# Kernel tuning notes

Measured on AMD Instinct MI355X. Metric: run time of the kernel, lower is better.

Reference implementation:

```python
import jax, jax.numpy as jnp
import numpy as np

N = {'QENT': 20000, 'CENT': 50000, 'SPAN': 40000, 'SENT': 40000}
E = 250000
IN_DIM, HID = 256, 128
NEG_SLOPE = 0.2  # GATConv default negative_slope
RELS = [('QENT', 'SPAN'), ('QENT', 'SENT'), ('CENT', 'SENT'), ('SPAN', 'CENT'), ('CENT', 'CENT')]
ENAMES = ['e_qent_span', 'e_qent_sent', 'e_cent_sent', 'e_span_cent', 'e_cent_cooccur']


def setup_inputs() -> dict:
    key = jax.random.key(0)
    ks = jax.random.split(key, 20)
    inp = {}
    for i, t in enumerate(['QENT', 'CENT', 'SPAN', 'SENT']):
        inp['x_' + t] = jax.random.normal(ks[i], (N[t], IN_DIM), jnp.float32)
    for i, (nm, (s, d)) in enumerate(zip(ENAMES, RELS)):
        k1, k2 = jax.random.split(ks[4 + i])
        src = jax.random.randint(k1, (E,), 0, N[s])
        dst = jax.random.randint(k2, (E,), 0, N[d])
        inp[nm] = jnp.stack([src, dst]).astype(jnp.int32)
    inp['lin_W'] = jax.random.normal(ks[10], (4, IN_DIM, HID), jnp.float32) / np.sqrt(IN_DIM).astype(np.float32)
    inp['lin_b'] = jnp.zeros((4, HID), jnp.float32)
    inp['conv_Ws'] = jax.random.normal(ks[11], (2, 5, HID, HID), jnp.float32) / np.sqrt(HID).astype(np.float32)
    inp['conv_Wd'] = jax.random.normal(ks[12], (2, 5, HID, HID), jnp.float32) / np.sqrt(HID).astype(np.float32)
    inp['conv_as'] = jax.random.normal(ks[13], (2, 5, HID), jnp.float32) / np.sqrt(HID).astype(np.float32)
    inp['conv_ad'] = jax.random.normal(ks[14], (2, 5, HID), jnp.float32) / np.sqrt(HID).astype(np.float32)
    inp['conv_b'] = jnp.zeros((2, 5, HID), jnp.float32)
    inp['out_W'] = jax.random.normal(ks[15], (HID, 1), jnp.float32) / np.sqrt(HID).astype(np.float32)
    inp['out_b'] = jnp.zeros((1,), jnp.float32)
    return inp


def _gat(x_src, x_dst, edge, Ws, Wd, a_s, a_d, b, n_dst):
    """PyG GATConv, heads=1, concat=True, add_self_loops=False, bipartite lin_src/lin_dst."""
    hs = x_src @ Ws                       # [Ns, H]
    hd = x_dst @ Wd                       # [Nd, H]
    src, dst = edge[0], edge[1]
    e = jax.nn.leaky_relu((hs @ a_s)[src] + (hd @ a_d)[dst], NEG_SLOPE)  # [E]
    m = jax.ops.segment_max(e, dst, num_segments=n_dst)
    m = jnp.where(jnp.isfinite(m), m, 0.0)
    ex = jnp.exp(e - m[dst])
    denom = jax.ops.segment_sum(ex, dst, num_segments=n_dst)
    alpha = ex / (denom[dst] + 1e-16)     # segment softmax (PyG adds 1e-16)
    out = jax.ops.segment_sum(alpha[:, None] * hs[src], dst, num_segments=n_dst)
    return out + b


def _forward(x_QENT, x_CENT, x_SPAN, x_SENT,
             e_qent_span, e_qent_sent, e_cent_sent, e_span_cent, e_cent_cooccur,
             lin_W, lin_b, conv_Ws, conv_Wd, conv_as, conv_ad, conv_b, out_W, out_b):
    # per-type input projection (pyg Linear has bias)
    x = {'QENT': x_QENT @ lin_W[0] + lin_b[0],
         'CENT': x_CENT @ lin_W[1] + lin_b[1],
         'SPAN': x_SPAN @ lin_W[2] + lin_b[2],
         'SENT': x_SENT @ lin_W[3] + lin_b[3]}
    for l in range(2):
        p = lambda r: (conv_Ws[l, r], conv_Wd[l, r], conv_as[l, r], conv_ad[l, r], conv_b[l, r])
        span = _gat(x['QENT'], x['SPAN'], e_qent_span, *p(0), N['SPAN'])
        sent = (_gat(x['QENT'], x['SENT'], e_qent_sent, *p(1), N['SENT'])
                + _gat(x['CENT'], x['SENT'], e_cent_sent, *p(2), N['SENT']))  # HeteroConv aggr='sum'
        cent = (_gat(x['SPAN'], x['CENT'], e_span_cent, *p(3), N['CENT'])
                + _gat(x['CENT'], x['CENT'], e_cent_cooccur, *p(4), N['CENT']))
        x = {'QENT': x['QENT'],  # QENT has no incoming edges; carried through so layer 2 can use it as source
             'SPAN': jax.nn.relu(span),
             'SENT': jax.nn.relu(sent),
             'CENT': jax.nn.relu(cent)}
    return (x['SPAN'] @ out_W + out_b)[:, 0]  # squeeze(-1) -> [N_SPAN]


def reference(x_QENT, x_CENT, x_SPAN, x_SENT,
              e_qent_span, e_qent_sent, e_cent_sent, e_span_cent, e_cent_cooccur,
              lin_W, lin_b, conv_Ws, conv_Wd, conv_as, conv_ad, conv_b, out_W, out_b):
    return _forward(x_QENT, x_CENT, x_SPAN, x_SENT,
                    e_qent_span, e_qent_sent, e_cent_sent, e_span_cent, e_cent_cooccur,
                    lin_W, lin_b, conv_Ws, conv_Wd, conv_as, conv_ad, conv_b, out_W, out_b)
```

## Files before the change

### kernel.cpp

```cpp
#include <hip/hip_runtime.h>
#include <hip/hip_fp16.h>

#define IN_DIM 256
#define HID 128
#define ELLW 16
#define OVF_CAP 32768

using bf16x8 = __attribute__((ext_vector_type(8))) short;
using f32x4 = __attribute__((ext_vector_type(4))) float;

struct h8 { __half2 a, b, c, d; };

__device__ __forceinline__ unsigned short f2bf(float f) {
    unsigned u = __float_as_uint(f);
    u += 0x7fffu + ((u >> 16) & 1u);
    return (unsigned short)(u >> 16);
}

template <int CTRL>
__device__ __forceinline__ float dpp_rot(float x) {
    return __int_as_float(
        __builtin_amdgcn_update_dpp(0, __float_as_int(x), CTRL, 0xf, 0xf, false));
}
__device__ __forceinline__ float rsum16(float x) {
    x += dpp_rot<0x121>(x);
    x += dpp_rot<0x122>(x);
    x += dpp_rot<0x124>(x);
    x += dpp_rot<0x128>(x);
    return x;
}
__device__ __forceinline__ float rmax16(float x) {
    x = fmaxf(x, dpp_rot<0x121>(x));
    x = fmaxf(x, dpp_rot<0x122>(x));
    x = fmaxf(x, dpp_rot<0x124>(x));
    x = fmaxf(x, dpp_rot<0x128>(x));
    return x;
}

__device__ __forceinline__ float lrelu(float t) { return t > 0.f ? t : 0.2f * t; }

__device__ __forceinline__ void accum8(f32x4& a0, f32x4& a1, float a, const h8& hv) {
    const float2 f0 = __half22float2(hv.a);
    const float2 f1 = __half22float2(hv.b);
    const float2 f2 = __half22float2(hv.c);
    const float2 f3 = __half22float2(hv.d);
    a0[0] += a * f0.x; a0[1] += a * f0.y;
    a0[2] += a * f1.x; a0[3] += a * f1.y;
    a1[0] += a * f2.x; a1[1] += a * f2.y;
    a1[2] += a * f3.x; a1[3] += a * f3.y;
}

__device__ __forceinline__ float epilogue16(const f32x4& a0, const f32x4& a1,
                                            const float* __restrict__ bias,
                                            const float* __restrict__ dvec, int sl) {
    const f32x4 bb0 = *reinterpret_cast<const f32x4*>(bias + sl * 8);
    const f32x4 bb1 = *reinterpret_cast<const f32x4*>(bias + sl * 8 + 4);
    const f32x4 d0 = *reinterpret_cast<const f32x4*>(dvec + sl * 8);
    const f32x4 d1 = *reinterpret_cast<const f32x4*>(dvec + sl * 8 + 4);
    float q = 0.f;
#pragma unroll
    for (int i = 0; i < 4; ++i) {
        q += fmaxf(a0[i] + bb0[i], 0.f) * d0[i];
        q += fmaxf(a1[i] + bb1[i], 0.f) * d1[i];
    }
    return rsum16(q);
}

__global__ __launch_bounds__(256) void setup_k(const float* __restrict__ lin_W,
                                               const float* __restrict__ lin_b,
                                               const float* __restrict__ conv_Ws,
                                               const float* __restrict__ Wd,
                                               const float* __restrict__ adv,
                                               short* __restrict__ wt0,
                                               short* __restrict__ wt1,
                                               float* __restrict__ bc,
                                               float* __restrict__ wd_out,
                                               float* __restrict__ v2,
                                               float* __restrict__ c2,
                                               int* __restrict__ deg,
                                               int* __restrict__ ell,
                                               int* __restrict__ ovf_cnt, int NS, int zd) {
    const int b = blockIdx.x;
    if (b < 256) {
        const int idx = b * 256 + threadIdx.x;
        const int l = idx >> 15;
        const int rem = idx & 32767;
        const int k = rem >> 7;
        const int n = rem & 127;
        const float* lw = lin_W + (size_t)k * HID;
        const float* cw = conv_Ws + (size_t)(l * 5) * HID * HID + n;
        float s = 0.f;
#pragma unroll 4
        for (int m = 0; m < HID; ++m) s += lw[m] * cw[(size_t)m * HID];
        short* wt = l ? wt1 : wt0;
        wt[((k >> 3) << 10) + (n << 3) + (k & 7)] = (short)f2bf(s);
    } else if (b == 256) {
        const int t = threadIdx.x;
        const int l = t >> 7;
        const int n = t & 127;
        const float* cw = conv_Ws + (size_t)(l * 5) * HID * HID + n;
        float s = 0.f;
#pragma unroll 4
        for (int m = 0; m < HID; ++m) s += lin_b[m] * cw[(size_t)m * HID];
        bc[t] = s;
        if (t == 0) ovf_cnt[0] = 0;
    } else if (b == 257) {
        __shared__ float wd1s[HID];
        const int t = threadIdx.x;
        const int l = t >> 7, j = t & 127;
        const float* w = Wd + ((size_t)(l * 5) * HID + j) * HID;
        const float* a = adv + (size_t)(l * 5) * HID;
        float s = 0.f;
        for (int k = 0; k < HID; k += 4) {
            const float4 wv = *reinterpret_cast<const float4*>(w + k);
            const float4 av = *reinterpret_cast<const float4*>(a + k);
            s += wv.x * av.x + wv.y * av.y + wv.z * av.z + wv.w * av.w;
        }
        wd_out[t] = s;
        if (l == 0) wd1s[j] = s;
        __syncthreads();
        const float* wr = lin_W + 2 * (size_t)IN_DIM * HID + (size_t)t * HID;
        float p = 0.f;
        for (int k = 0; k < HID; k += 4) {
            const float4 wv = *reinterpret_cast<const float4*>(wr + k);
            p += wv.x * wd1s[k] + wv.y * wd1s[k + 1] + wv.z * wd1s[k + 2] +
                 wv.w * wd1s[k + 3];
        }
        v2[t] = p;
        if (t == 0) {
            const float* br = lin_b + 2 * HID;
            float q = 0.f;
            for (int k = 0; k < HID; ++k) q += br[k] * wd1s[k];
            c2[0] = q;
        }
    } else if (b < 258 + zd) {
        const int i4 = ((b - 258) * 256 + threadIdx.x) * 4;
        if (i4 + 4 <= NS) {
            *reinterpret_cast<int4*>(deg + i4) = make_int4(0, 0, 0, 0);
        } else {
            for (int i = i4; i < NS; ++i) deg[i] = 0;
        }
    } else {
        const int total = NS * ELLW;
        const int i4 = ((b - 258 - zd) * 256 + threadIdx.x) * 4;
        if (i4 + 4 <= total) *reinterpret_cast<int4*>(ell + i4) = make_int4(0, 0, 0, 0);
    }
}

__global__ __launch_bounds__(256) void build_gemm_k(
    const int* __restrict__ src, const int* __restrict__ dst, int E,
    int* __restrict__ deg, int* __restrict__ ell, int2* __restrict__ ovf,
    int* __restrict__ ovf_cnt, const float* __restrict__ A,
    const short* __restrict__ Wt0, const short* __restrict__ Wt1,
    const float* __restrict__ bc, __half* __restrict__ hs,
    float2* __restrict__ as12, const float* __restrict__ a1v,
    const float* __restrict__ a2v, int N, int eb) {
    if ((int)blockIdx.x < eb) {
        const int e = blockIdx.x * 256 + threadIdx.x;
        if (e < E) {
            const int d = dst[e], s = src[e];
            const int pos = atomicAdd(deg + d, 1);
            if (pos < ELLW) {
                ell[(size_t)d * ELLW + pos] = s;
            } else {
                const int oi = atomicAdd(ovf_cnt, 1);
                if (oi < OVF_CAP) ovf[oi] = make_int2(d, s);
            }
        }
        return;
    }
    const int bid = (int)blockIdx.x - eb;
    const int tid = threadIdx.x;
    const int w = tid >> 6;
    const int lane = tid & 63;
    const int m16 = lane & 15;
    const int kg = lane >> 4;

    const int arow = bid * 64 + w * 16 + m16;
    const bool ok = arow < N;

    f32x4 acc[16];
#pragma unroll
    for (int j = 0; j < 16; ++j) acc[j] = (f32x4){0.f, 0.f, 0.f, 0.f};

    for (int k0 = 0; k0 < IN_DIM; k0 += 32) {
        bf16x8 af = {0, 0, 0, 0, 0, 0, 0, 0};
        if (ok) {
            const float* ap = A + (size_t)arow * IN_DIM + k0 + kg * 8;
            const float4 f0 = *reinterpret_cast<const float4*>(ap);
            const float4 f1 = *reinterpret_cast<const float4*>(ap + 4);
            af[0] = (short)f2bf(f0.x); af[1] = (short)f2bf(f0.y);
            af[2] = (short)f2bf(f0.z); af[3] = (short)f2bf(f0.w);
            af[4] = (short)f2bf(f1.x); af[5] = (short)f2bf(f1.y);
            af[6] = (short)f2bf(f1.z); af[7] = (short)f2bf(f1.w);
        }
        const int boff = ((k0 >> 3) + kg) << 10;
        const short* b0 = Wt0 + boff;
        const short* b1 = Wt1 + boff;
#pragma unroll
        for (int j = 0; j < 8; ++j) {
            const bf16x8 bf0 = *reinterpret_cast<const bf16x8*>(b0 + ((j * 16 + m16) << 3));
            acc[j] = __builtin_amdgcn_mfma_f32_16x16x32_bf16(af, bf0, acc[j], 0, 0, 0);
            const bf16x8 bf1 = *reinterpret_cast<const bf16x8*>(b1 + ((j * 16 + m16) << 3));
            acc[j + 8] = __builtin_amdgcn_mfma_f32_16x16x32_bf16(af, bf1, acc[j + 8], 0, 0, 0);
        }
    }

    const int rbase = bid * 64 + w * 16 + kg * 4;
    float p1[4] = {0.f, 0.f, 0.f, 0.f};
    float p2[4] = {0.f, 0.f, 0.f, 0.f};
#pragma unroll
    for (int j = 0; j < 8; ++j) {
        const int col = j * 16 + m16;
        const float b0v = bc[col];
        const float b1v = bc[128 + col];
        const float a1 = a1v[col];
        const float a2 = a2v[col];
        const int so = j * 32 + ((m16 >> 3) << 4) + (m16 & 7);
#pragma unroll
        for (int r = 0; r < 4; ++r) {
            const int row = rbase + r;
            const float v1 = acc[j][r] + b0v;
            const float v2v = acc[j + 8][r] + b1v;
            if (row < N) {
                hs[(size_t)row * 256 + so] = __float2half(v1);
                hs[(size_t)row * 256 + so + 8] = __float2half(v2v);
            }
            p1[r] += v1 * a1;
            p2[r] += v2v * a2;
        }
    }
#pragma unroll
    for (int r = 0; r < 4; ++r) {
        p1[r] = rsum16(p1[r]);
        p2[r] = rsum16(p2[r]);
    }
    if (m16 == 0)
#pragma unroll
        for (int r = 0; r < 4; ++r) {
            const int row = rbase + r;
            if (row < N) as12[row] = make_float2(p1[r], p2[r]);
        }
}

__global__ __launch_bounds__(256, 4) void gat_fused_k(
    const int* __restrict__ deg_arr, const int* __restrict__ ell,
    const int2* __restrict__ ovf, const int* __restrict__ ovf_cnt_p,
    const float* __restrict__ x_span, const float* __restrict__ v2,
    const float* __restrict__ c2, const float2* __restrict__ as12,
    const __half* __restrict__ hs, const float* __restrict__ b1,
    const float* __restrict__ wd2v, const float* __restrict__ b2,
    const float* __restrict__ outW, const float* __restrict__ outb,
    float* __restrict__ out, int Ndst) {
    const int gidx = blockIdx.x * blockDim.x + threadIdx.x;
    const int row = gidx >> 4;
    const int sl = threadIdx.x & 15;
    const int grp = threadIdx.x & 48;
    if (row >= Ndst) return;

    const int deg = deg_arr[row];
    const int ce = ell[(size_t)row * ELLW + sl];

    float p = 0.f;
    const float* xr = x_span + (size_t)row * IN_DIM + sl * 16;
    const float* vr = v2 + sl * 16;
#pragma unroll
    for (int i = 0; i < 4; ++i) {
        const float4 xv = *reinterpret_cast<const float4*>(xr + i * 4);
        const float4 vv = *reinterpret_cast<const float4*>(vr + i * 4);
        p += xv.x * vv.x + xv.y * vv.y + xv.z * vv.z + xv.w * vv.w;
    }
    const float ad1 = rsum16(p) + c2[0];

    const float2 asv = as12[ce];
    const float a1c = asv.x;
    const float a2c = asv.y;

    h8 h1[8], h2[8];
#pragma unroll
    for (int i = 0; i < 8; ++i) {
        const int s = __shfl(ce, grp | i, 64);
        const __half* hb = hs + (size_t)s * 256 + sl * 16;
        h1[i] = *reinterpret_cast<const h8*>(hb);
        h2[i] = *reinterpret_cast<const h8*>(hb + 8);
    }

    if (deg <= ELLW) {
        const float ex1 = (sl < deg) ? __expf(lrelu(a1c + ad1)) : 0.f;
        const float al1 = ex1 / (rsum16(ex1) + 1e-16f);

        f32x4 acc0 = {0.f, 0.f, 0.f, 0.f}, acc1 = {0.f, 0.f, 0.f, 0.f};
#pragma unroll
        for (int i = 0; i < 8; ++i) {
            const float a = __shfl(al1, grp | i, 64);
            accum8(acc0, acc1, a, h1[i]);
        }
        for (int i = 8; i < deg; ++i) {
            const int s = __shfl(ce, grp | i, 64);
            const float a = __shfl(al1, grp | i, 64);
            const h8 hv = *reinterpret_cast<const h8*>(hs + (size_t)s * 256 + sl * 16);
            accum8(acc0, acc1, a, hv);
        }
        const float ad2 = epilogue16(acc0, acc1, b1, wd2v, sl);

        const float ex2 = (sl < deg) ? __expf(lrelu(a2c + ad2)) : 0.f;
        const float al2 = ex2 / (rsum16(ex2) + 1e-16f);

        f32x4 bcc0 = {0.f, 0.f, 0.f, 0.f}, bcc1 = {0.f, 0.f, 0.f, 0.f};
#pragma unroll
        for (int i = 0; i < 8; ++i) {
            const float a = __shfl(al2, grp | i, 64);
            accum8(bcc0, bcc1, a, h2[i]);
        }
        for (int i = 8; i < deg; ++i) {
            const int s = __shfl(ce, grp | i, 64);
            const float a = __shfl(al2, grp | i, 64);
            const h8 hv = *reinterpret_cast<const h8*>(hs + (size_t)s * 256 + sl * 16 + 8);
            accum8(bcc0, bcc1, a, hv);
        }
        const float q = epilogue16(bcc0, bcc1, b2, outW, sl);
        if (sl == 0) out[row] = q + outb[0];
    } else {
        int oc = *ovf_cnt_p;
        if (oc > OVF_CAP) oc = OVF_CAP;
        float ad = ad1;
#pragma unroll
        for (int layer = 0; layer < 2; ++layer) {
            const float ac = layer ? a2c : a1c;
            const int ho = layer ? 8 : 0;
            const float* bias = layer ? b2 : b1;
            const float* dvec = layer ? outW : wd2v;

            float te = lrelu(ac + ad);
            float m = rmax16(te);
            for (int i = 0; i < oc; ++i) {
                const int2 o = ovf[i];
                if (o.x == row) {
                    const float2 oas = as12[o.y];
                    m = fmaxf(m, lrelu((layer ? oas.y : oas.x) + ad));
                }
            }
            const float ex = __expf(te - m);
            float dsum = rsum16(ex);
            for (int i = 0; i < oc; ++i) {
                const int2 o = ovf[i];
                if (o.x == row) {
                    const float2 oas = as12[o.y];
                    dsum += __expf(lrelu((layer ? oas.y : oas.x) + ad) - m);
                }
            }
            const float inv = 1.f / (dsum + 1e-16f);
            const float al = ex * inv;

            f32x4 acc0 = {0.f, 0.f, 0.f, 0.f}, acc1 = {0.f, 0.f, 0.f, 0.f};
#pragma unroll
            for (int i = 0; i < 16; ++i) {
                const int s = __shfl(ce, grp | i, 64);
                const float a = __shfl(al, grp | i, 64);
                const h8 hv =
                    *reinterpret_cast<const h8*>(hs + (size_t)s * 256 + sl * 16 + ho);
                accum8(acc0, acc1, a, hv);
            }
            for (int i = 0; i < oc; ++i) {
                const int2 o = ovf[i];
                if (o.x == row) {
                    const float2 oas = as12[o.y];
                    const float a = __expf(lrelu((layer ? oas.y : oas.x) + ad) - m) * inv;
                    const h8 hv =
                        *reinterpret_cast<const h8*>(hs + (size_t)o.y * 256 + sl * 16 + ho);
                    accum8(acc0, acc1, a, hv);
                }
            }
            const float q = epilogue16(acc0, acc1, bias, dvec, sl);
            if (layer == 0) {
                ad = q;
            } else if (sl == 0) {
                out[row] = q + outb[0];
            }
        }
    }
}

extern "C" void kernel_launch(void* const* d_in, const int* in_sizes, int n_in,
                              void* d_out, int out_size, void* d_ws, size_t ws_size,
                              hipStream_t stream) {
    const float* x_qent = (const float*)d_in[0];
    const float* x_span = (const float*)d_in[2];
    const int* e_qs = (const int*)d_in[4];
    const float* lin_W = (const float*)d_in[9];
    const float* lin_b = (const float*)d_in[10];
    const float* conv_Ws = (const float*)d_in[11];
    const float* conv_Wd = (const float*)d_in[12];
    const float* conv_as = (const float*)d_in[13];
    const float* conv_ad = (const float*)d_in[14];
    const float* conv_b = (const float*)d_in[15];
    const float* out_W = (const float*)d_in[16];
    const float* out_b = (const float*)d_in[17];

    const int NQ = in_sizes[0] / IN_DIM;
    const int NS = in_sizes[2] / IN_DIM;
    const int E = in_sizes[4] / 2;
    const int* srcp = e_qs;
    const int* dstp = e_qs + E;
    (void)n_in; (void)out_size;

    float* ws = (float*)d_ws;
    size_t off = 0;
    auto alloc = [&](size_t n) {
        n = (n + 3) & ~(size_t)3;
        float* p = ws + off;
        off += n;
        return p;
    };
    __half* hs = (__half*)alloc((size_t)NQ * 128);
    float2* as12 = (float2*)alloc(2 * (size_t)NQ);
    float* wd2 = alloc(2 * HID);
    float* v2 = alloc(IN_DIM);
    float* c2 = alloc(1);
    float* bc = alloc(2 * HID);
    int* deg = (int*)alloc(NS);
    int* ell = (int*)alloc((size_t)NS * ELLW);
    int2* ovf = (int2*)alloc(2 * OVF_CAP);
    int* ovf_cnt = (int*)alloc(1);
    short* wt0 = (short*)alloc(IN_DIM * HID / 2);
    short* wt1 = (short*)alloc(IN_DIM * HID / 2);
    (void)ws_size;

    const int zd = (NS + 1023) / 1024;
    const int ze = (NS * ELLW + 1023) / 1024;
    setup_k<<<dim3(258 + zd + ze), dim3(256), 0, stream>>>(
        lin_W, lin_b, conv_Ws, conv_Wd, conv_ad, wt0, wt1, bc, wd2, v2, c2, deg, ell,
        ovf_cnt, NS, zd);

    const int eb = (E + 255) / 256;
    const int gb = (NQ + 63) / 64;
    build_gemm_k<<<dim3(eb + gb), dim3(256), 0, stream>>>(
        srcp, dstp, E, deg, ell, ovf, ovf_cnt, x_qent, wt0, wt1, bc, hs, as12, conv_as,
        conv_as + 5 * (size_t)HID, NQ, eb);

    gat_fused_k<<<dim3(((size_t)NS * 16 + 255) / 256), dim3(256), 0, stream>>>(
        deg, ell, ovf, ovf_cnt, x_span, v2, c2, as12, hs, conv_b, wd2 + HID,
        conv_b + 5 * (size_t)HID, out_W, out_b, (float*)d_out, NS);
}
```

Measured before the change: 86.63 us.

## Assign one wavefront per destination row, splitting edges across four lane groups

The fused GAT kernel now maps a full 64-lane wavefront to each SPAN row instead of 16 lanes. The four 16-lane groups each handle every fourth neighbour and combine partial sums with xor shuffles. The x·v dot product is also spread over 64 lanes. The aim is more memory-level parallelism and fewer serial gather steps per row, at the cost of four times as many threads, extra cross-lane reductions, and idle lanes when degree is low.

```diff
diff --git a/kernel.cpp b/kernel.cpp
--- a/kernel.cpp
+++ b/kernel.cpp
@@ -252,81 +252,79 @@
     const float* __restrict__ wd2v, const float* __restrict__ b2,
     const float* __restrict__ outW, const float* __restrict__ outb,
     float* __restrict__ out, int Ndst) {
-    const int gidx = blockIdx.x * blockDim.x + threadIdx.x;
-    const int row = gidx >> 4;
-    const int sl = threadIdx.x & 15;
-    const int grp = threadIdx.x & 48;
+    const int row = (blockIdx.x * blockDim.x + threadIdx.x) >> 6;
+    const int lane = threadIdx.x & 63;
+    const int sl = lane & 15;
+    const int eg = lane >> 4;
     if (row >= Ndst) return;
 
     const int deg = deg_arr[row];
     const int ce = ell[(size_t)row * ELLW + sl];
-
-    float p = 0.f;
-    const float* xr = x_span + (size_t)row * IN_DIM + sl * 16;
-    const float* vr = v2 + sl * 16;
-#pragma unroll
-    for (int i = 0; i < 4; ++i) {
-        const float4 xv = *reinterpret_cast<const float4*>(xr + i * 4);
-        const float4 vv = *reinterpret_cast<const float4*>(vr + i * 4);
-        p += xv.x * vv.x + xv.y * vv.y + xv.z * vv.z + xv.w * vv.w;
-    }
-    const float ad1 = rsum16(p) + c2[0];
-
     const float2 asv = as12[ce];
-    const float a1c = asv.x;
-    const float a2c = asv.y;
-
-    h8 h1[8], h2[8];
-#pragma unroll
-    for (int i = 0; i < 8; ++i) {
-        const int s = __shfl(ce, grp | i, 64);
-        const __half* hb = hs + (size_t)s * 256 + sl * 16;
-        h1[i] = *reinterpret_cast<const h8*>(hb);
-        h2[i] = *reinterpret_cast<const h8*>(hb + 8);
-    }
+
+    const float4 xv = *reinterpret_cast<const float4*>(x_span + (size_t)row * IN_DIM +
+                                                       lane * 4);
+    const float4 vv = *reinterpret_cast<const float4*>(v2 + lane * 4);
+    float p = xv.x * vv.x + xv.y * vv.y + xv.z * vv.z + xv.w * vv.w;
+    p = rsum16(p);
+    p += __shfl_xor(p, 16, 64);
+    p += __shfl_xor(p, 32, 64);
+    const float ad1 = p + c2[0];
 
     if (deg <= ELLW) {
-        const float ex1 = (sl < deg) ? __expf(lrelu(a1c + ad1)) : 0.f;
+        const float ex1 = (sl < deg) ? __expf(lrelu(asv.x + ad1)) : 0.f;
         const float al1 = ex1 / (rsum16(ex1) + 1e-16f);
 
-        f32x4 acc0 = {0.f, 0.f, 0.f, 0.f}, acc1 = {0.f, 0.f, 0.f, 0.f};
-#pragma unroll
-        for (int i = 0; i < 8; ++i) {
-            const float a = __shfl(al1, grp | i, 64);
-            accum8(acc0, acc1, a, h1[i]);
-        }
-        for (int i = 8; i < deg; ++i) {
-            const int s = __shfl(ce, grp | i, 64);
-            const float a = __shfl(al1, grp | i, 64);
-            const h8 hv = *reinterpret_cast<const h8*>(hs + (size_t)s * 256 + sl * 16);
-            accum8(acc0, acc1, a, hv);
-        }
-        const float ad2 = epilogue16(acc0, acc1, b1, wd2v, sl);
-
-        const float ex2 = (sl < deg) ? __expf(lrelu(a2c + ad2)) : 0.f;
+        f32x4 a0 = {0.f, 0.f, 0.f, 0.f}, a1 = {0.f, 0.f, 0.f, 0.f};
+        h8 h2s[4];
+#pragma unroll
+        for (int r = 0; r < 4; ++r) {
+            if (r * 4 < deg) {
+                const int e = r * 4 + eg;
+                const int s = __shfl(ce, e, 64);
+                const float a = __shfl(al1, e, 64);
+                const __half* hb = hs + (size_t)s * 256 + sl * 16;
+                const h8 hv1 = *reinterpret_cast<const h8*>(hb);
+                h2s[r] = *reinterpret_cast<const h8*>(hb + 8);
+                accum8(a0, a1, a, hv1);
+            }
+        }
+#pragma unroll
+        for (int i = 0; i < 4; ++i) {
+            a0[i] += __shfl_xor(a0[i], 16, 64);
+            a0[i] += __shfl_xor(a0[i], 32, 64);
+            a1[i] += __shfl_xor(a1[i], 16, 64);
+            a1[i] += __shfl_xor(a1[i], 32, 64);
+        }
+        const float ad2 = epilogue16(a0, a1, b1, wd2v, sl);
+
+        const float ex2 = (sl < deg) ? __expf(lrelu(asv.y + ad2)) : 0.f;
         const float al2 = ex2 / (rsum16(ex2) + 1e-16f);
 
-        f32x4 bcc0 = {0.f, 0.f, 0.f, 0.f}, bcc1 = {0.f, 0.f, 0.f, 0.f};
-#pragma unroll
-        for (int i = 0; i < 8; ++i) {
-            const float a = __shfl(al2, grp | i, 64);
-            accum8(bcc0, bcc1, a, h2[i]);
-        }
-        for (int i = 8; i < deg; ++i) {
-            const int s = __shfl(ce, grp | i, 64);
-            const float a = __shfl(al2, grp | i, 64);
-            const h8 hv = *reinterpret_cast<const h8*>(hs + (size_t)s * 256 + sl * 16 + 8);
-            accum8(bcc0, bcc1, a, hv);
-        }
-        const float q = epilogue16(bcc0, bcc1, b2, outW, sl);
-        if (sl == 0) out[row] = q + outb[0];
+        f32x4 b0 = {0.f, 0.f, 0.f, 0.f}, b1v = {0.f, 0.f, 0.f, 0.f};
+#pragma unroll
+        for (int r = 0; r < 4; ++r) {
+            if (r * 4 < deg) {
+                const float a = __shfl(al2, r * 4 + eg, 64);
+                accum8(b0, b1v, a, h2s[r]);
+            }
+        }
+#pragma unroll
+        for (int i = 0; i < 4; ++i) {
+            b0[i] += __shfl_xor(b0[i], 16, 64);
+            b0[i] += __shfl_xor(b0[i], 32, 64);
+            b1v[i] += __shfl_xor(b1v[i], 16, 64);
+            b1v[i] += __shfl_xor(b1v[i], 32, 64);
+        }
+        const float q = epilogue16(b0, b1v, b2, outW, sl);
+        if (lane == 0) out[row] = q + outb[0];
     } else {
         int oc = *ovf_cnt_p;
         if (oc > OVF_CAP) oc = OVF_CAP;
         float ad = ad1;
 #pragma unroll
         for (int layer = 0; layer < 2; ++layer) {
-            const float ac = layer ? a2c : a1c;
+            const float ac = layer ? asv.y : asv.x;
             const int ho = layer ? 8 : 0;
             const float* bias = layer ? b2 : b1;
             const float* dvec = layer ? outW : wd2v;
@@ -353,17 +351,17 @@
             const float al = ex * inv;
 
             f32x4 acc0 = {0.f, 0.f, 0.f, 0.f}, acc1 = {0.f, 0.f, 0.f, 0.f};
-#pragma unroll
             for (int i = 0; i < 16; ++i) {
-                const int s = __shfl(ce, grp | i, 64);
-                const float a = __shfl(al, grp | i, 64);
+                const int s = __shfl(ce, i, 64);
+                float a = __shfl(al, i, 64);
+                if (eg != 0) a = 0.f;
                 const h8 hv =
                     *reinterpret_cast<const h8*>(hs + (size_t)s * 256 + sl * 16 + ho);
                 accum8(acc0, acc1, a, hv);
             }
             for (int i = 0; i < oc; ++i) {
                 const int2 o = ovf[i];
-                if (o.x == row) {
+                if (o.x == row && eg == 0) {
                     const float2 oas = as12[o.y];
                     const float a = __expf(lrelu((layer ? oas.y : oas.x) + ad) - m) * inv;
                     const h8 hv =
@@ -371,10 +369,17 @@
                     accum8(acc0, acc1, a, hv);
                 }
             }
+#pragma unroll
+            for (int i = 0; i < 4; ++i) {
+                acc0[i] += __shfl_xor(acc0[i], 16, 64);
+                acc0[i] += __shfl_xor(acc0[i], 32, 64);
+                acc1[i] += __shfl_xor(acc1[i], 16, 64);
+                acc1[i] += __shfl_xor(acc1[i], 32, 64);
+            }
             const float q = epilogue16(acc0, acc1, bias, dvec, sl);
             if (layer == 0) {
                 ad = q;
-            } else if (sl == 0) {
+            } else if (lane == 0) {
                 out[row] = q + outb[0];
             }
         }
@@ -438,7 +443,7 @@
         srcp, dstp, E, deg, ell, ovf, ovf_cnt, x_qent, wt0, wt1, bc, hs, as12, conv_as,
         conv_as + 5 * (size_t)HID, NQ, eb);
 
-    gat_fused_k<<<dim3(((size_t)NS * 16 + 255) / 256), dim3(256), 0, stream>>>(
+    gat_fused_k<<<dim3(((size_t)NS * 64 + 255) / 256), dim3(256), 0, stream>>>(
         deg, ell, ovf, ovf_cnt, x_span, v2, c2, as12, hs, conv_b, wd2 + HID,
         conv_b + 5 * (size_t)HID, out_W, out_b, (float*)d_out, NS);
 }
```

Measured after the change: 88.10 us. Within noise of the previous version (+1.7%).
